# Kernel tuning notes

Hardware: AMD Instinct MI355X
Metric: run time of the kernel (lower is better)

## Reference

```python
import jax, jax.numpy as jnp
import numpy as np
from jax import lax

T_MAX, BATCH, CLASSES, L_MAX = 512, 32, 1296, 64
NINF = -jnp.inf


def _align_one(logsm, label, C, R):
    """Monotonic max-probability forced alignment for one sample.
    logsm: [T, V] log-probs, label: [L] int, C=x_len (valid frames), R=label_len.
    Returns per-frame pseudo target [T] (0-padded past C)."""
    T, V = logsm.shape
    L = label.shape[0]
    rows = jnp.arange(L)
    cols = jnp.arange(T)
    # pb[i, j] = logsm[j, label[i]], restricted to the monotonic band i <= j <= C-R+i
    pb = logsm[:, label].T  # [L, T]
    band = (cols[None, :] >= rows[:, None]) & (cols[None, :] <= C - R + rows[:, None]) & (rows[:, None] < R)
    pb = jnp.where(band, pb, NINF)

    # Forward DP over time columns: dp[i,j] = max(dp[i-1,j-1], dp[i,j-1]) + pb[i,j]
    # (strict > for the diagonal move, exactly as the original numpy code).
    dp0 = jnp.where(rows == 0, pb[:, 0], NINF)

    def step(dp, pb_col):
        shifted = jnp.concatenate([jnp.full((1,), NINF, dp.dtype), dp[:-1]])
        choice = shifted > dp  # True -> came from (i-1, j-1)
        dp_new = jnp.where(choice, shifted, dp) + pb_col
        return dp_new, choice

    _, choices = lax.scan(step, dp0, pb.T[1:])  # [T-1, L] bool
    choices = jnp.concatenate([jnp.zeros((1, L), bool), choices], axis=0)  # [T, L]

    # Backtrack from (R-1, C-1); columns j >= C emit padding 0.
    def bstep(row, jc):
        j, ch = jc
        active = j < C
        tgt = jnp.where(active, label[row], 0)
        row_new = jnp.where(active, row - ch[row].astype(row.dtype), row)
        return row_new, tgt

    row0 = (R - 1).astype(jnp.int32)
    _, targets = lax.scan(bstep, row0, (jnp.arange(T), choices), reverse=True)
    return targets  # [T]


def _make_targets(logsm, label, x_len, label_len):
    # logsm: [T, B, V] -> targets [T, B]
    return jax.vmap(_align_one, in_axes=(1, 0, 0, 0))(logsm, label, x_len, label_len).T


def setup_inputs() -> dict:
    key = jax.random.key(0)
    k0, k1, k2, k3, k4 = jax.random.split(key, 5)
    pred = jax.random.normal(k0, (T_MAX, BATCH, CLASSES), jnp.float32)
    seq_pred = jax.random.normal(k1, (T_MAX, BATCH, CLASSES), jnp.float32)
    label = jax.random.randint(k2, (BATCH, L_MAX), 0, CLASSES)
    x_len = jax.random.randint(k3, (BATCH,), T_MAX // 2, T_MAX + 1)  # >= L_MAX so band is valid
    label_len = jax.random.randint(k4, (BATCH,), 8, L_MAX + 1)
    return {"pred": pred, "seq_pred": seq_pred, "label": label, "x_len": x_len, "label_len": label_len}


def reference(pred, seq_pred, label, x_len, label_len):
    T, B, V = pred.shape
    logsm_seq = jax.nn.log_softmax(seq_pred, axis=-1)
    target = _make_targets(logsm_seq, label, x_len, label_len)  # [T, B] int
    probs = jnp.exp(logsm_seq)  # softmax(seq_pred)
    conf = jnp.take_along_axis(probs, target[..., None], axis=2)[..., 0]  # [T, B]
    smooth = (1.0 - conf) / (V - 1)
    onehot = jax.nn.one_hot(target, V, dtype=pred.dtype)  # [T, B, V]
    true_dist = jnp.where(onehot > 0, conf[..., None], smooth[..., None])
    mask = (jnp.arange(T)[:, None] < x_len[None, :]).astype(pred.dtype)  # [T, B]
    ce = jnp.sum(-true_dist * jax.nn.log_softmax(pred, axis=-1), axis=-1) * mask
    return jnp.mean(ce)
```

## Files before the change

kernel.cpp:

```cpp
#include <hip/hip_runtime.h>

#define T_MAX 512
#define BATCH 32
#define CLASSES 1296
#define L_MAX 64
#define NROWS (T_MAX * BATCH)
#define NINF (-INFINITY)
#define ALIGNBLK 4

__device__ __forceinline__ float wave_sum64(float v) {
    v += __int_as_float(__builtin_amdgcn_update_dpp(0, __float_as_int(v), 0x111, 0xF, 0xF, true));
    v += __int_as_float(__builtin_amdgcn_update_dpp(0, __float_as_int(v), 0x112, 0xF, 0xF, true));
    v += __int_as_float(__builtin_amdgcn_update_dpp(0, __float_as_int(v), 0x114, 0xF, 0xF, true));
    v += __int_as_float(__builtin_amdgcn_update_dpp(0, __float_as_int(v), 0x118, 0xF, 0xF, true));
    v += __int_as_float(__builtin_amdgcn_update_dpp(0, __float_as_int(v), 0x142, 0xF, 0xF, true));
    v += __int_as_float(__builtin_amdgcn_update_dpp(0, __float_as_int(v), 0x143, 0xF, 0xF, true));
    return v;
}

__global__ __launch_bounds__(256) void seq_rowstats_kernel(
    const float* __restrict__ seqp, const int* __restrict__ label,
    float* __restrict__ lse_seq, float* __restrict__ pb, int* __restrict__ counter)
{
    int r = blockIdx.x * 4 + (threadIdx.x >> 6);
    int lane = threadIdx.x & 63;
    if (r == 0 && lane == 0) *counter = 0;
    const float* xs = seqp + (size_t)r * CLASSES;
    const float4* s4 = (const float4*)xs;

    float4 b0 = s4[lane],       b1 = s4[lane + 64],  b2 = s4[lane + 128];
    float4 b3 = s4[lane + 192], b4 = s4[lane + 256];
    float4 bt = make_float4(0.f, 0.f, 0.f, 0.f);
    if (lane < 4) bt = s4[320 + lane];
    int lab = label[((r & 31) << 6) + lane];

    float ss = __expf(b0.x) + __expf(b0.y) + __expf(b0.z) + __expf(b0.w)
             + __expf(b1.x) + __expf(b1.y) + __expf(b1.z) + __expf(b1.w)
             + __expf(b2.x) + __expf(b2.y) + __expf(b2.z) + __expf(b2.w)
             + __expf(b3.x) + __expf(b3.y) + __expf(b3.z) + __expf(b3.w)
             + __expf(b4.x) + __expf(b4.y) + __expf(b4.z) + __expf(b4.w);
    if (lane < 4)
        ss += __expf(bt.x) + __expf(bt.y) + __expf(bt.z) + __expf(bt.w);
    ss = wave_sum64(ss);

    int b = r & 31, t = r >> 5;
    pb[(((size_t)(b << 9) + t) << 6) + lane] = xs[lab];
    if (lane == 63) lse_seq[r] = __logf(ss);
}

__global__ __launch_bounds__(512, 3) void fused_align_pred_kernel(
    const float* __restrict__ pred, const float* __restrict__ pb,
    const int* __restrict__ x_len, const int* __restrict__ label_len,
    float* __restrict__ lse_pred, float* __restrict__ sum_pred,
    int* __restrict__ tg)
{
    __shared__ unsigned chw[8][1024];
    __shared__ int a_s[8][64];
    __shared__ int rows_s[8][T_MAX];
    const int w = threadIdx.x >> 6, lane = threadIdx.x & 63;

    if (blockIdx.x < ALIGNBLK) {
        const int b = (blockIdx.x << 3) + w;
        const int C = x_len[b], R = label_len[b];
        const int limit = C - R;
        const float* pbb = pb + ((size_t)b << 15);
        const int P = (C + 31) >> 5;
        const float biasR = (lane < R) ? 0.f : NINF;
        const bool isb0 = (lane & 15) == 0;
        const int ninf_i = 0xFF800000;
        unsigned* chwl = chw[w];

        float va[16], vb[16];
        float dp = NINF;
        unsigned w0 = 0;

#define GLOAD(VV, GG) {                                                        \
        const float* s_ = pbb + ((size_t)(GG) << 10);                          \
        _Pragma("unroll")                                                      \
        for (int u = 0; u < 16; ++u) VV[u] = s_[(u << 6) + lane];              \
    }

#define COMPUTE16(VV, GG) {                                                    \
        const int g_ = (GG);                                                   \
        const bool general = (g_ < 2) || (((g_ << 4) + 15) > limit);           \
        _Pragma("unroll")                                                      \
        for (int u = 0; u < 16; ++u) {                                         \
            const int j = (g_ << 4) + u;                                       \
            float val;                                                         \
            if (general) {                                                     \
                if (g_ == 0 && u == 0) {                    \
                    dp = (lane == 0) ? VV[0] : NINF;                           \
                    continue;                                                  \
                }                                                              \
                const bool ib = (lane <= j) && (lane >= j - limit) && (lane < R); \
                val = ib ? VV[u] : NINF;                                       \
            } else {                                                           \
                val = VV[u] + biasR;                     \
            }                                                                  \
            const int dpb = __float_as_int(dp);                                \
            const int t1 = __builtin_amdgcn_update_dpp(ninf_i, dpb, 0x111, 0xF, 0xF, false);  \
            const int t2 = __builtin_amdgcn_update_dpp(ninf_i, dpb, 0x142, 0xF, 0xF, false);  \
            const float shifted = __int_as_float(isb0 ? t2 : t1);              \
            const bool c = shifted > dp;                \
            w0 |= (c ? 1u : 0u) << (j & 31);                                   \
            dp = fmaxf(shifted, dp) + val;            \
        }                                                                      \
    }

        GLOAD(va, 0)
        for (int p = 0; p < P; ++p) {
            const int g0 = p << 1;
            GLOAD(vb, g0 + 1)
            w0 = 0;
            COMPUTE16(va, g0)
            if (p + 1 < P) GLOAD(va, g0 + 2)
            COMPUTE16(vb, g0 + 1)
            chwl[(p << 6) + lane] = w0;
        }
#undef GLOAD
#undef COMPUTE16

        if (lane == 0) {
            int row = R - 1, j = C - 1;
            while (row > 0 && j >= 0) {
                unsigned word = chwl[((j >> 5) << 6) + row];
                unsigned mb = (2u << (j & 31)) - 1;
                unsigned m = word & mb;
                if (m) {
                    int hb = 31 - __clz(m);
                    int aj = (j & ~31) | hb;
                    a_s[w][row] = aj;
                    row--; j = aj - 1;
                } else {
                    j = (j & ~31) - 1;
                }
            }
            for (int i = row; i >= 0; --i) a_s[w][i] = 0;
        }
        if (lane < R) {
            int a = a_s[w][lane];
            int bi = (lane == R - 1) ? (C - 1) : (a_s[w][lane + 1] - 1);
            for (int j = a; j <= bi; ++j) rows_s[w][j] = lane;
        }
        for (int j = lane; j < T_MAX; j += 64)
            tg[(b << 9) + j] = (j < C) ? rows_s[w][j] : -1;
    } else {
        const int r = ((blockIdx.x - ALIGNBLK) << 3) + w;
        const float* xp = pred + (size_t)r * CLASSES;
        const float4* p4 = (const float4*)xp;

        float4 a0 = p4[lane],       a1 = p4[lane + 64],  a2 = p4[lane + 128];
        float4 a3 = p4[lane + 192], a4 = p4[lane + 256];
        float4 at = make_float4(0.f, 0.f, 0.f, 0.f);
        if (lane < 4) at = p4[320 + lane];

        float sp = __expf(a0.x) + __expf(a0.y) + __expf(a0.z) + __expf(a0.w)
                 + __expf(a1.x) + __expf(a1.y) + __expf(a1.z) + __expf(a1.w)
                 + __expf(a2.x) + __expf(a2.y) + __expf(a2.z) + __expf(a2.w)
                 + __expf(a3.x) + __expf(a3.y) + __expf(a3.z) + __expf(a3.w)
                 + __expf(a4.x) + __expf(a4.y) + __expf(a4.z) + __expf(a4.w);
        float sx = (a0.x + a0.y + a0.z + a0.w) + (a1.x + a1.y + a1.z + a1.w)
                 + (a2.x + a2.y + a2.z + a2.w) + (a3.x + a3.y + a3.z + a3.w)
                 + (a4.x + a4.y + a4.z + a4.w);
        if (lane < 4) {
            sp += __expf(at.x) + __expf(at.y) + __expf(at.z) + __expf(at.w);
            sx += at.x + at.y + at.z + at.w;
        }
        sp = wave_sum64(sp);
        sx = wave_sum64(sx);
        if (lane == 63) {
            lse_pred[r] = __logf(sp);
            sum_pred[r] = sx;
        }
    }
}

__global__ __launch_bounds__(256) void ce_kernel(
    const float* __restrict__ pred, const int* __restrict__ label,
    const int* __restrict__ x_len,
    const float* __restrict__ lse_pred, const float* __restrict__ sum_pred,
    const float* __restrict__ lse_seq, const float* __restrict__ pb,
    const int* __restrict__ tg, float* __restrict__ partials,
    int* __restrict__ counter, float* __restrict__ out)
{
    int e = blockIdx.x * 256 + threadIdx.x;
    int t = e >> 5, b = e & 31;
    float ce = 0.f;
    if (t < x_len[b]) {
        int row = tg[(b << 9) + t];
        int tgt = label[(b << 6) + row];
        float lp = lse_pred[e];
        float S = sum_pred[e] - (float)CLASSES * lp;
        float lsp_t = pred[(size_t)e * CLASSES + tgt] - lp;
        float conf = __expf(pb[(((size_t)(b << 9) + t) << 6) + row] - lse_seq[e]);
        float smooth = (1.f - conf) * (1.f / (float)(CLASSES - 1));
        ce = -((conf - smooth) * lsp_t + smooth * S);
    }
    ce = wave_sum64(ce);
    __shared__ float sm[4];
    __shared__ int amLast;
    if ((threadIdx.x & 63) == 63) sm[threadIdx.x >> 6] = ce;
    __syncthreads();
    if (threadIdx.x == 0) {
        float p = sm[0] + sm[1] + sm[2] + sm[3];
        __hip_atomic_store(&partials[blockIdx.x], p, __ATOMIC_RELEASE, __HIP_MEMORY_SCOPE_AGENT);
        amLast = (__hip_atomic_fetch_add(counter, 1, __ATOMIC_ACQ_REL, __HIP_MEMORY_SCOPE_AGENT) == 63);
    }
    __syncthreads();
    if (amLast && threadIdx.x < 64) {
        float v = __hip_atomic_load(&partials[threadIdx.x], __ATOMIC_ACQUIRE, __HIP_MEMORY_SCOPE_AGENT);
        for (int o = 32; o; o >>= 1) v += __shfl_down(v, o, 64);
        if (threadIdx.x == 0) out[0] = v * (1.0f / (float)NROWS);
    }
}

extern "C" void kernel_launch(void* const* d_in, const int* in_sizes, int n_in,
                              void* d_out, int out_size, void* d_ws, size_t ws_size,
                              hipStream_t stream) {
    const float* pred      = (const float*)d_in[0];
    const float* seq_pred  = (const float*)d_in[1];
    const int*   label     = (const int*)d_in[2];
    const int*   x_len     = (const int*)d_in[3];
    const int*   label_len = (const int*)d_in[4];
    float* out = (float*)d_out;

    float* ws = (float*)d_ws;
    float* lse_pred = ws;
    float* sum_pred = ws + NROWS;
    float* lse_seq  = ws + 2 * NROWS;
    float* pb       = ws + 3 * NROWS;
    int*   tg       = (int*)(pb + (size_t)BATCH * T_MAX * 64);
    float* partials = (float*)(tg + NROWS);
    int*   counter  = (int*)(partials + 64);

    seq_rowstats_kernel<<<NROWS / 4, 256, 0, stream>>>(seq_pred, label,
                                                       lse_seq, pb, counter);
    fused_align_pred_kernel<<<ALIGNBLK + NROWS / 8, 512, 0, stream>>>(
        pred, pb, x_len, label_len, lse_pred, sum_pred, tg);
    ce_kernel<<<64, 256, 0, stream>>>(pred, label, x_len,
                                      lse_pred, sum_pred, lse_seq, pb, tg,
                                      partials, counter, out);
}
```

Measured before the change: 213.0 us.

## Fuse both softmax row passes, fold CE into the alignment kernel, prefetch deeper

Row statistics for seq_pred and pred are now computed together in one streaming kernel. The seq_pred label gather reads from a row staged in shared memory instead of re-reading global memory. The alignment DP moves into its own 4-block kernel with a four-buffer prefetch of the band probabilities, and it computes the cross-entropy terms and the final reduction directly, which removes the separate CE kernel and the tg buffer. The cost is that the serial alignment no longer overlaps the pred streaming pass and must wait for it to finish.

```diff
diff --git a/kernel.cpp b/kernel.cpp
--- a/kernel.cpp
+++ b/kernel.cpp
@@ -6,7 +6,8 @@
 #define L_MAX 64
 #define NROWS (T_MAX * BATCH)
 #define NINF (-INFINITY)
-#define ALIGNBLK 4
+#define NSEQBLK (NROWS / 8)
+#define NPREDBLK (NROWS / 8)
 
 __device__ __forceinline__ float wave_sum64(float v) {
     v += __int_as_float(__builtin_amdgcn_update_dpp(0, __float_as_int(v), 0x111, 0xF, 0xF, true));
@@ -18,64 +19,109 @@
     return v;
 }
 
-__global__ __launch_bounds__(256) void seq_rowstats_kernel(
-    const float* __restrict__ seqp, const int* __restrict__ label,
-    float* __restrict__ lse_seq, float* __restrict__ pb, int* __restrict__ counter)
+__global__ __launch_bounds__(512, 4) void stream_kernel(
+    const float* __restrict__ pred, const float* __restrict__ seqp,
+    const int* __restrict__ label,
+    float* __restrict__ lse_pred, float* __restrict__ sum_pred,
+    float* __restrict__ lse_seq, float* __restrict__ pb,
+    int* __restrict__ counter)
 {
-    int r = blockIdx.x * 4 + (threadIdx.x >> 6);
-    int lane = threadIdx.x & 63;
-    if (r == 0 && lane == 0) *counter = 0;
-    const float* xs = seqp + (size_t)r * CLASSES;
-    const float4* s4 = (const float4*)xs;
-
-    float4 b0 = s4[lane],       b1 = s4[lane + 64],  b2 = s4[lane + 128];
-    float4 b3 = s4[lane + 192], b4 = s4[lane + 256];
-    float4 bt = make_float4(0.f, 0.f, 0.f, 0.f);
-    if (lane < 4) bt = s4[320 + lane];
-    int lab = label[((r & 31) << 6) + lane];
-
-    float ss = __expf(b0.x) + __expf(b0.y) + __expf(b0.z) + __expf(b0.w)
-             + __expf(b1.x) + __expf(b1.y) + __expf(b1.z) + __expf(b1.w)
-             + __expf(b2.x) + __expf(b2.y) + __expf(b2.z) + __expf(b2.w)
-             + __expf(b3.x) + __expf(b3.y) + __expf(b3.z) + __expf(b3.w)
-             + __expf(b4.x) + __expf(b4.y) + __expf(b4.z) + __expf(b4.w);
-    if (lane < 4)
-        ss += __expf(bt.x) + __expf(bt.y) + __expf(bt.z) + __expf(bt.w);
-    ss = wave_sum64(ss);
-
-    int b = r & 31, t = r >> 5;
-    pb[(((size_t)(b << 9) + t) << 6) + lane] = xs[lab];
-    if (lane == 63) lse_seq[r] = __logf(ss);
-}
-
-__global__ __launch_bounds__(512, 3) void fused_align_pred_kernel(
+    __shared__ float rowbuf[8][CLASSES];
+    const int w = threadIdx.x >> 6, lane = threadIdx.x & 63;
+    if (blockIdx.x == 0 && threadIdx.x == 0) *counter = 0;
+
+    if (blockIdx.x < NSEQBLK) {
+        const int r = (blockIdx.x << 3) + w;
+        const int b = r & 31, t = r >> 5;
+        const float* xs = seqp + (size_t)r * CLASSES;
+        const float4* s4 = (const float4*)xs;
+
+        float4 b0 = s4[lane],       b1 = s4[lane + 64],  b2 = s4[lane + 128];
+        float4 b3 = s4[lane + 192], b4 = s4[lane + 256];
+        float4 bt = make_float4(0.f, 0.f, 0.f, 0.f);
+        if (lane < 4) bt = s4[320 + lane];
+        const int lab = label[(b << 6) + lane];
+
+        float4* rb4 = (float4*)rowbuf[w];
+        rb4[lane] = b0; rb4[lane + 64] = b1; rb4[lane + 128] = b2;
+        rb4[lane + 192] = b3; rb4[lane + 256] = b4;
+        if (lane < 4) rb4[320 + lane] = bt;
+
+        float ss = __expf(b0.x) + __expf(b0.y) + __expf(b0.z) + __expf(b0.w)
+                 + __expf(b1.x) + __expf(b1.y) + __expf(b1.z) + __expf(b1.w)
+                 + __expf(b2.x) + __expf(b2.y) + __expf(b2.z) + __expf(b2.w)
+                 + __expf(b3.x) + __expf(b3.y) + __expf(b3.z) + __expf(b3.w)
+                 + __expf(b4.x) + __expf(b4.y) + __expf(b4.z) + __expf(b4.w);
+        if (lane < 4)
+            ss += __expf(bt.x) + __expf(bt.y) + __expf(bt.z) + __expf(bt.w);
+        ss = wave_sum64(ss);
+        if (lane == 63) lse_seq[r] = __logf(ss);
+
+        pb[(((size_t)(b << 9) + t) << 6) + lane] = rowbuf[w][lab];
+    } else {
+        const int r = ((blockIdx.x - NSEQBLK) << 3) + w;
+        const float* xp = pred + (size_t)r * CLASSES;
+        const float4* p4 = (const float4*)xp;
+
+        float4 a0 = p4[lane],       a1 = p4[lane + 64],  a2 = p4[lane + 128];
+        float4 a3 = p4[lane + 192], a4 = p4[lane + 256];
+        float4 at = make_float4(0.f, 0.f, 0.f, 0.f);
+        if (lane < 4) at = p4[320 + lane];
+
+        float sp = __expf(a0.x) + __expf(a0.y) + __expf(a0.z) + __expf(a0.w)
+                 + __expf(a1.x) + __expf(a1.y) + __expf(a1.z) + __expf(a1.w)
+                 + __expf(a2.x) + __expf(a2.y) + __expf(a2.z) + __expf(a2.w)
+                 + __expf(a3.x) + __expf(a3.y) + __expf(a3.z) + __expf(a3.w)
+                 + __expf(a4.x) + __expf(a4.y) + __expf(a4.z) + __expf(a4.w);
+        float sx = (a0.x + a0.y + a0.z + a0.w) + (a1.x + a1.y + a1.z + a1.w)
+                 + (a2.x + a2.y + a2.z + a2.w) + (a3.x + a3.y + a3.z + a3.w)
+                 + (a4.x + a4.y + a4.z + a4.w);
+        if (lane < 4) {
+            sp += __expf(at.x) + __expf(at.y) + __expf(at.z) + __expf(at.w);
+            sx += at.x + at.y + at.z + at.w;
+        }
+        sp = wave_sum64(sp);
+        sx = wave_sum64(sx);
+        if (lane == 63) {
+            lse_pred[r] = __logf(sp);
+            sum_pred[r] = sx;
+        }
+    }
+}
+
+__global__ __launch_bounds__(512, 2) void align_ce_kernel(
     const float* __restrict__ pred, const float* __restrict__ pb,
-    const int* __restrict__ x_len, const int* __restrict__ label_len,
-    float* __restrict__ lse_pred, float* __restrict__ sum_pred,
-    int* __restrict__ tg)
+    const int* __restrict__ label, const int* __restrict__ x_len,
+    const int* __restrict__ label_len,
+    const float* __restrict__ lse_pred, const float* __restrict__ sum_pred,
+    const float* __restrict__ lse_seq,
+    float* __restrict__ partials, int* __restrict__ counter,
+    float* __restrict__ out)
 {
     __shared__ unsigned chw[8][1024];
     __shared__ int a_s[8][64];
     __shared__ int rows_s[8][T_MAX];
+    __shared__ float sm[8];
     const int w = threadIdx.x >> 6, lane = threadIdx.x & 63;
 
-    if (blockIdx.x < ALIGNBLK) {
-        const int b = (blockIdx.x << 3) + w;
-        const int C = x_len[b], R = label_len[b];
-        const int limit = C - R;
-        const float* pbb = pb + ((size_t)b << 15);
-        const int P = (C + 31) >> 5;
-        const float biasR = (lane < R) ? 0.f : NINF;
-        const bool isb0 = (lane & 15) == 0;
-        const int ninf_i = 0xFF800000;
-        unsigned* chwl = chw[w];
-
-        float va[16], vb[16];
-        float dp = NINF;
-        unsigned w0 = 0;
+    const int b = (blockIdx.x << 3) + w;
+    const int C = x_len[b], R = label_len[b];
+    const int limit = C - R;
+    const float* pbb = pb + ((size_t)b << 15);
+    const int P = (C + 31) >> 5;
+    const int G = P << 1;
+    const float biasR = (lane < R) ? 0.f : NINF;
+    const bool isb0 = (lane & 15) == 0;
+    const int ninf_i = 0xFF800000;
+    unsigned* chwl = chw[w];
+
+    float bA[16], bB[16], bC[16], bD[16];
+    float dp = NINF;
+    unsigned w0 = 0;
 
 #define GLOAD(VV, GG) {                                                        \
-        const float* s_ = pbb + ((size_t)(GG) << 10);                          \
+        int gi_ = (GG); if (gi_ > G - 1) gi_ = G - 1;                          \
+        const float* s_ = pbb + ((size_t)gi_ << 10);                           \
         _Pragma("unroll")                                                      \
         for (int u = 0; u < 16; ++u) VV[u] = s_[(u << 6) + lane];              \
     }
@@ -107,110 +153,75 @@
         }                                                                      \
     }
 
-        GLOAD(va, 0)
-        for (int p = 0; p < P; ++p) {
-            const int g0 = p << 1;
-            GLOAD(vb, g0 + 1)
-            w0 = 0;
-            COMPUTE16(va, g0)
-            if (p + 1 < P) GLOAD(va, g0 + 2)
-            COMPUTE16(vb, g0 + 1)
-            chwl[(p << 6) + lane] = w0;
-        }
+    GLOAD(bA, 0) GLOAD(bB, 1) GLOAD(bC, 2)
+    for (int g = 0; g < G; g += 4) {
+        GLOAD(bD, g + 3)
+        COMPUTE16(bA, g)
+        GLOAD(bA, g + 4)
+        COMPUTE16(bB, g + 1)
+        chwl[((g >> 1) << 6) + lane] = w0; w0 = 0;
+        if (g + 2 < G) {
+            GLOAD(bB, g + 5)
+            COMPUTE16(bC, g + 2)
+            GLOAD(bC, g + 6)
+            COMPUTE16(bD, g + 3)
+            chwl[(((g >> 1) + 1) << 6) + lane] = w0; w0 = 0;
+        }
+    }
 #undef GLOAD
 #undef COMPUTE16
 
-        if (lane == 0) {
-            int row = R - 1, j = C - 1;
-            while (row > 0 && j >= 0) {
-                unsigned word = chwl[((j >> 5) << 6) + row];
-                unsigned mb = (2u << (j & 31)) - 1;
-                unsigned m = word & mb;
-                if (m) {
-                    int hb = 31 - __clz(m);
-                    int aj = (j & ~31) | hb;
-                    a_s[w][row] = aj;
-                    row--; j = aj - 1;
-                } else {
-                    j = (j & ~31) - 1;
-                }
+    if (lane == 0) {
+        int row = R - 1, j = C - 1;
+        while (row > 0 && j >= 0) {
+            unsigned word = chwl[((j >> 5) << 6) + row];
+            unsigned mb = (2u << (j & 31)) - 1;
+            unsigned m = word & mb;
+            if (m) {
+                int hb = 31 - __clz(m);
+                int aj = (j & ~31) | hb;
+                a_s[w][row] = aj;
+                row--; j = aj - 1;
+            } else {
+                j = (j & ~31) - 1;
             }
-            for (int i = row; i >= 0; --i) a_s[w][i] = 0;
-        }
-        if (lane < R) {
-            int a = a_s[w][lane];
-            int bi = (lane == R - 1) ? (C - 1) : (a_s[w][lane + 1] - 1);
-            for (int j = a; j <= bi; ++j) rows_s[w][j] = lane;
-        }
-        for (int j = lane; j < T_MAX; j += 64)
-            tg[(b << 9) + j] = (j < C) ? rows_s[w][j] : -1;
-    } else {
-        const int r = ((blockIdx.x - ALIGNBLK) << 3) + w;
-        const float* xp = pred + (size_t)r * CLASSES;
-        const float4* p4 = (const float4*)xp;
-
-        float4 a0 = p4[lane],       a1 = p4[lane + 64],  a2 = p4[lane + 128];
-        float4 a3 = p4[lane + 192], a4 = p4[lane + 256];
-        float4 at = make_float4(0.f, 0.f, 0.f, 0.f);
-        if (lane < 4) at = p4[320 + lane];
-
-        float sp = __expf(a0.x) + __expf(a0.y) + __expf(a0.z) + __expf(a0.w)
-                 + __expf(a1.x) + __expf(a1.y) + __expf(a1.z) + __expf(a1.w)
-                 + __expf(a2.x) + __expf(a2.y) + __expf(a2.z) + __expf(a2.w)
-                 + __expf(a3.x) + __expf(a3.y) + __expf(a3.z) + __expf(a3.w)
-                 + __expf(a4.x) + __expf(a4.y) + __expf(a4.z) + __expf(a4.w);
-        float sx = (a0.x + a0.y + a0.z + a0.w) + (a1.x + a1.y + a1.z + a1.w)
-                 + (a2.x + a2.y + a2.z + a2.w) + (a3.x + a3.y + a3.z + a3.w)
-                 + (a4.x + a4.y + a4.z + a4.w);
-        if (lane < 4) {
-            sp += __expf(at.x) + __expf(at.y) + __expf(at.z) + __expf(at.w);
-            sx += at.x + at.y + at.z + at.w;
-        }
-        sp = wave_sum64(sp);
-        sx = wave_sum64(sx);
-        if (lane == 63) {
-            lse_pred[r] = __logf(sp);
-            sum_pred[r] = sx;
-        }
-    }
-}
-
-__global__ __launch_bounds__(256) void ce_kernel(
-    const float* __restrict__ pred, const int* __restrict__ label,
-    const int* __restrict__ x_len,
-    const float* __restrict__ lse_pred, const float* __restrict__ sum_pred,
-    const float* __restrict__ lse_seq, const float* __restrict__ pb,
-    const int* __restrict__ tg, float* __restrict__ partials,
-    int* __restrict__ counter, float* __restrict__ out)
-{
-    int e = blockIdx.x * 256 + threadIdx.x;
-    int t = e >> 5, b = e & 31;
-    float ce = 0.f;
-    if (t < x_len[b]) {
-        int row = tg[(b << 9) + t];
-        int tgt = label[(b << 6) + row];
-        float lp = lse_pred[e];
-        float S = sum_pred[e] - (float)CLASSES * lp;
-        float lsp_t = pred[(size_t)e * CLASSES + tgt] - lp;
-        float conf = __expf(pb[(((size_t)(b << 9) + t) << 6) + row] - lse_seq[e]);
-        float smooth = (1.f - conf) * (1.f / (float)(CLASSES - 1));
-        ce = -((conf - smooth) * lsp_t + smooth * S);
-    }
-    ce = wave_sum64(ce);
-    __shared__ float sm[4];
-    __shared__ int amLast;
-    if ((threadIdx.x & 63) == 63) sm[threadIdx.x >> 6] = ce;
+        }
+        for (int i = row; i >= 0; --i) a_s[w][i] = 0;
+    }
+    if (lane < R) {
+        int a = a_s[w][lane];
+        int bi = (lane == R - 1) ? (C - 1) : (a_s[w][lane + 1] - 1);
+        for (int j = a; j <= bi; ++j) rows_s[w][j] = lane;
+    }
+
+    float ces = 0.f;
+    #pragma unroll
+    for (int k = 0; k < 8; ++k) {
+        const int t = (k << 6) + lane;
+        if (t < C) {
+            const int e = (t << 5) + b;
+            const int row = rows_s[w][t];
+            const int tgt = label[(b << 6) + row];
+            const float lp = lse_pred[e];
+            const float S = sum_pred[e] - (float)CLASSES * lp;
+            const float lsp_t = pred[(size_t)e * CLASSES + tgt] - lp;
+            const float conf = __expf(pb[(((size_t)(b << 9) + t) << 6) + row] - lse_seq[e]);
+            const float smooth = (1.f - conf) * (1.f / (float)(CLASSES - 1));
+            ces += -((conf - smooth) * lsp_t + smooth * S);
+        }
+    }
+    ces = wave_sum64(ces);
+    if (lane == 63) sm[w] = ces;
     __syncthreads();
     if (threadIdx.x == 0) {
-        float p = sm[0] + sm[1] + sm[2] + sm[3];
+        float p = sm[0] + sm[1] + sm[2] + sm[3] + sm[4] + sm[5] + sm[6] + sm[7];
         __hip_atomic_store(&partials[blockIdx.x], p, __ATOMIC_RELEASE, __HIP_MEMORY_SCOPE_AGENT);
-        amLast = (__hip_atomic_fetch_add(counter, 1, __ATOMIC_ACQ_REL, __HIP_MEMORY_SCOPE_AGENT) == 63);
-    }
-    __syncthreads();
-    if (amLast && threadIdx.x < 64) {
-        float v = __hip_atomic_load(&partials[threadIdx.x], __ATOMIC_ACQUIRE, __HIP_MEMORY_SCOPE_AGENT);
-        for (int o = 32; o; o >>= 1) v += __shfl_down(v, o, 64);
-        if (threadIdx.x == 0) out[0] = v * (1.0f / (float)NROWS);
+        if (__hip_atomic_fetch_add(counter, 1, __ATOMIC_ACQ_REL, __HIP_MEMORY_SCOPE_AGENT) == 3) {
+            float v = 0.f;
+            for (int i = 0; i < 4; ++i)
+                v += __hip_atomic_load(&partials[i], __ATOMIC_ACQUIRE, __HIP_MEMORY_SCOPE_AGENT);
+            out[0] = v * (1.0f / (float)NROWS);
+        }
     }
 }
 
@@ -229,15 +240,12 @@
     float* sum_pred = ws + NROWS;
     float* lse_seq  = ws + 2 * NROWS;
     float* pb       = ws + 3 * NROWS;
-    int*   tg       = (int*)(pb + (size_t)BATCH * T_MAX * 64);
-    float* partials = (float*)(tg + NROWS);
-    int*   counter  = (int*)(partials + 64);
-
-    seq_rowstats_kernel<<<NROWS / 4, 256, 0, stream>>>(seq_pred, label,
-                                                       lse_seq, pb, counter);
-    fused_align_pred_kernel<<<ALIGNBLK + NROWS / 8, 512, 0, stream>>>(
-        pred, pb, x_len, label_len, lse_pred, sum_pred, tg);
-    ce_kernel<<<64, 256, 0, stream>>>(pred, label, x_len,
-                                      lse_pred, sum_pred, lse_seq, pb, tg,
-                                      partials, counter, out);
-}
+    float* partials = pb + (size_t)BATCH * T_MAX * 64;
+    int*   counter  = (int*)(partials + 4);
+
+    stream_kernel<<<NSEQBLK + NPREDBLK, 512, 0, stream>>>(
+        pred, seq_pred, label, lse_pred, sum_pred, lse_seq, pb, counter);
+    align_ce_kernel<<<4, 512, 0, stream>>>(
+        pred, pb, label, x_len, label_len,
+        lse_pred, sum_pred, lse_seq, partials, counter, out);
+}
```

Result: slower. 232.5 us (+9.2%).
